# Kernel optimization log

Hardware: AMD Instinct MI355X
Metric: run time of the kernel (lower is better)

The kernel has to match this reference:

```python
import jax, jax.numpy as jnp
import numpy as np

EPS = 1e-6
K = 20
NUM_OBJECTS = 50
OBJ_FEAT = 256
C_DIM = 128
HIDDEN = 128


def vn_linear(x, W):
    # x: [B, C, 3, ...]; W: [O, C] -> [B, O, 3, ...]
    return jnp.einsum('oc,bc...->bo...', W, x)


def vn_leaky(x, Wdir, slope):
    d = vn_linear(x, Wdir)
    dot = jnp.sum(x * d, axis=2, keepdims=True)
    dsq = jnp.sum(d * d, axis=2, keepdims=True)
    x_neg = x - (dot / (dsq + EPS)) * d
    return slope * x + (1.0 - slope) * jnp.where(dot >= 0, x, x_neg)


def vn_linear_leaky(x, Wfeat, Wdir, slope):
    pf = vn_linear(x, Wfeat)
    d = vn_linear(x, Wdir)
    dot = jnp.sum(pf * d, axis=2, keepdims=True)
    dsq = jnp.sum(d * d, axis=2, keepdims=True)
    p_neg = pf - (dot / (dsq + EPS)) * d
    return slope * pf + (1.0 - slope) * jnp.where(dot >= 0, pf, p_neg)


def resblock(x, fc0, fc1, a0, a1, sc):
    net = vn_linear(vn_leaky(x, a0, 0.0), fc0)
    dx = vn_linear(vn_leaky(net, a1, 0.0), fc1)
    return vn_linear(x, sc) + dx


def get_graph_feature_cross(x, k):
    # x: [B, 3, N] -> edge features [B, 3, 3, N, k]
    inner = -2.0 * jnp.einsum('bdn,bdm->bnm', x, x)
    xx = jnp.sum(x * x, axis=1)                       # [B, N]
    neg_dist = -xx[:, :, None] - inner - xx[:, None, :]  # [B, N, N]
    idx = jax.lax.top_k(neg_dist, k)[1]               # [B, N, k] nearest neighbors
    xt = jnp.transpose(x, (0, 2, 1))                  # [B, N, 3]
    nbr = jax.vmap(lambda pts, ind: pts[ind])(xt, idx)  # [B, N, k, 3]
    ctr = jnp.broadcast_to(xt[:, :, None, :], nbr.shape)
    cross = jnp.cross(nbr, ctr)
    feat = jnp.stack([nbr - ctr, ctr, cross], axis=3)  # [B, N, k, 3, 3]
    return jnp.transpose(feat, (0, 3, 4, 1, 2))


def mlp2(zf, w0, w1, w2):
    h = jax.nn.relu(zf @ w0.T)
    h = jax.nn.relu(h @ w1.T)
    return h @ w2.T


def setup_inputs():
    key = jax.random.key(0)
    ks = jax.random.split(key, 24)
    B, N = 4, 4096

    def rn(k, shape):
        return jax.random.normal(k, shape, dtype=jnp.float32) * (1.0 / np.sqrt(shape[-1]))

    return {
        'p': jax.random.normal(ks[0], (B, N, 3), dtype=jnp.float32),
        'z_idxs': jax.random.randint(ks[1], (B,), 0, NUM_OBJECTS),
        'z': jax.random.normal(ks[2], (NUM_OBJECTS, OBJ_FEAT), dtype=jnp.float32),
        'hw0': rn(ks[3], (OBJ_FEAT, OBJ_FEAT)),
        'hw1': rn(ks[4], (OBJ_FEAT, OBJ_FEAT)),
        'hw2': rn(ks[5], (C_DIM * HIDDEN, OBJ_FEAT)),
        'hb0': rn(ks[6], (OBJ_FEAT, OBJ_FEAT)),
        'hb1': rn(ks[7], (OBJ_FEAT, OBJ_FEAT)),
        'hb2': rn(ks[8], (C_DIM, OBJ_FEAT)),
        'conv_pos_feat': rn(ks[9], (128, 3)),
        'conv_pos_dir': rn(ks[10], (128, 3)),
        'fc_pos_w': rn(ks[11], (2 * HIDDEN, 128)),
        'blk_fc0': rn(ks[12], (5, HIDDEN, 2 * HIDDEN)),
        'blk_fc1': rn(ks[13], (5, HIDDEN, HIDDEN)),
        'blk_act0': rn(ks[14], (5, 2 * HIDDEN, 2 * HIDDEN)),
        'blk_act1': rn(ks[15], (5, HIDDEN, HIDDEN)),
        'blk_sc': rn(ks[16], (5, HIDDEN, 2 * HIDDEN)),
        'actc_dir': rn(ks[17], (HIDDEN, HIDDEN)),
    }


def reference(p, z_idxs, z, hw0, hw1, hw2, hb0, hb1, hb2, conv_pos_feat,
              conv_pos_dir, fc_pos_w, blk_fc0, blk_fc1, blk_act0, blk_act1,
              blk_sc, actc_dir):
    B = p.shape[0]
    x = jnp.transpose(p, (0, 2, 1))                       # [B, 3, N]
    feat = get_graph_feature_cross(x, K)                  # [B, 3, 3, N, k]
    net = vn_linear_leaky(feat, conv_pos_feat, conv_pos_dir, 0.2)  # [B,128,3,N,k]
    net = jnp.mean(net, axis=-1)                          # [B,128,3,N]
    net = vn_linear(net, fc_pos_w)                        # [B,256,3,N]
    for i in range(5):
        net = resblock(net, blk_fc0[i], blk_fc1[i], blk_act0[i], blk_act1[i], blk_sc[i])
        if i < 4:
            pooled = jnp.mean(net, axis=-1, keepdims=True)
            net = jnp.concatenate([net, jnp.broadcast_to(pooled, net.shape)], axis=1)
    net = vn_leaky(jnp.mean(net, axis=-1), actc_dir, 0.2)  # [B, HIDDEN, 3]
    zf = z[z_idxs]                                        # [B, OBJ_FEAT]
    w = mlp2(zf, hw0, hw1, hw2).reshape(B, C_DIM, HIDDEN)  # hypernet weights
    b = mlp2(zf, hb0, hb1, hb2)                           # [B, C_DIM]
    c = jnp.einsum('bhd,bch->bcd', net, w) + b[:, :, None]  # [B, C_DIM, 3]
    return c
```

## Files before the change

### kernel.cpp

```cpp
#include <hip/hip_runtime.h>
#include <hip/hip_fp16.h>
#include <cstdint>
#include <cstddef>

#define NPTS 4096
#define BATCH 4
#define KNN 20

typedef __half f16;
using f32x4 = __attribute__((ext_vector_type(4))) float;
using f16x8 = __attribute__((ext_vector_type(8))) _Float16;

__global__ __launch_bounds__(256) void knn_kernel(const float* __restrict__ p,
                                                  int* __restrict__ idx_out) {
    __shared__ float pts[12288];
    const int tid  = threadIdx.x;
    const int wave = tid >> 6, lane = tid & 63;
    const int b  = blockIdx.x >> 10;
    const int nb = ((blockIdx.x & 1023) << 2) + wave;

    const float4* src4 = (const float4*)(p + (size_t)b * NPTS * 3);
    float4* dst4 = (float4*)pts;
    for (int i = tid; i < NPTS * 3 / 4; i += 256) dst4[i] = src4[i];
    __syncthreads();

    const float cx = pts[3 * nb], cy = pts[3 * nb + 1], cz = pts[3 * nb + 2];
    unsigned lst[4];
#pragma unroll
    for (int i = 0; i < 4; i++) lst[i] = 0xFFFFFFFFu;

    for (int t = 0; t < NPTS / 64; t++) {
        int m = (t << 6) + lane;
        float dx = pts[3 * m] - cx, dy = pts[3 * m + 1] - cy, dz = pts[3 * m + 2] - cz;
        float d = dx * dx + dy * dy + dz * dz;
        unsigned c = (__float_as_uint(d) & 0xFFFFF000u) | (unsigned)m;
#pragma unroll
        for (int j = 0; j < 4; j++) {
            unsigned lo = min(c, lst[j]);
            c = max(c, lst[j]);
            lst[j] = lo;
        }
    }

    unsigned lo = 0u, hi = 0xFFFFFFFFu;
    for (int it = 0; it < 32; it++) {
        unsigned mid = lo + ((hi - lo) >> 1);
        int cnt = __popcll(__ballot(lst[0] <= mid)) + __popcll(__ballot(lst[1] <= mid))
                + __popcll(__ballot(lst[2] <= mid)) + __popcll(__ballot(lst[3] <= mid));
        if (cnt >= KNN) hi = mid; else lo = mid + 1;
    }
    const unsigned T = hi;

    unsigned long long bl[4];
#pragma unroll
    for (int j = 0; j < 4; j++) bl[j] = __ballot(lst[j] <= T);
    const unsigned long long lmask = (lane == 63) ? ~0ull >> 1 : (1ull << lane) - 1;
    int base = 0;
    const size_t out_base = ((size_t)b * NPTS + nb) * KNN;
#pragma unroll
    for (int j = 0; j < 4; j++) {
        if (lst[j] <= T) {
            int pos = base + (int)__popcll(bl[j] & lmask);
            idx_out[out_base + pos] = (int)(lst[j] & 0xFFFu);
        }
        base += (int)__popcll(bl[j]);
    }
}

__global__ __launch_bounds__(128) void edgeconv_kernel(
    const float* __restrict__ p, const int* __restrict__ idx,
    const float* __restrict__ wf, const float* __restrict__ wd,
    f16* __restrict__ out) {
    __shared__ float e[KNN][6];
    const int col = blockIdx.x;
    const int b = col >> 12;
    const int tid = threadIdx.x;
    const float cx = p[(size_t)col * 3], cy = p[(size_t)col * 3 + 1], cz = p[(size_t)col * 3 + 2];
    if (tid < KNN) {
        int j = idx[(size_t)col * KNN + tid];
        const float* q = &p[((size_t)b * NPTS + j) * 3];
        float nx = q[0], ny = q[1], nz = q[2];
        e[tid][0] = nx - cx; e[tid][1] = ny - cy; e[tid][2] = nz - cz;
        e[tid][3] = ny * cz - nz * cy;
        e[tid][4] = nz * cx - nx * cz;
        e[tid][5] = nx * cy - ny * cx;
    }
    __syncthreads();
    const int o = tid;
    const float f0 = wf[o * 3], f1 = wf[o * 3 + 1], f2 = wf[o * 3 + 2];
    const float g0 = wd[o * 3], g1 = wd[o * 3 + 1], g2 = wd[o * 3 + 2];
    const float pc0 = f1 * cx, pc1 = f1 * cy, pc2 = f1 * cz;
    const float gc0 = g1 * cx, gc1 = g1 * cy, gc2 = g1 * cz;
    float a0 = 0.f, a1 = 0.f, a2 = 0.f;
    for (int k = 0; k < KNN; k++) {
        float d0 = e[k][0], d1 = e[k][1], d2 = e[k][2];
        float c0 = e[k][3], c1 = e[k][4], c2 = e[k][5];
        float pf0 = fmaf(f0, d0, fmaf(f2, c0, pc0));
        float pf1 = fmaf(f0, d1, fmaf(f2, c1, pc1));
        float pf2 = fmaf(f0, d2, fmaf(f2, c2, pc2));
        float dd0 = fmaf(g0, d0, fmaf(g2, c0, gc0));
        float dd1 = fmaf(g0, d1, fmaf(g2, c1, gc1));
        float dd2 = fmaf(g0, d2, fmaf(g2, c2, gc2));
        float dot = pf0 * dd0 + pf1 * dd1 + pf2 * dd2;
        float dsq = dd0 * dd0 + dd1 * dd1 + dd2 * dd2;
        float w = 0.8f * dot * __builtin_amdgcn_rcpf(dsq + 1e-6f);
        w = (dot >= 0.f) ? 0.f : w;
        a0 += pf0 - w * dd0;
        a1 += pf1 - w * dd1;
        a2 += pf2 - w * dd2;
    }
    const float inv = 1.f / (float)KNN;
    out[((size_t)col * 3 + 0) * 128 + o] = __float2half(a0 * inv);
    out[((size_t)col * 3 + 1) * 128 + o] = __float2half(a1 * inv);
    out[((size_t)col * 3 + 2) * 128 + o] = __float2half(a2 * inv);
}

template <int KIN>
__global__ __launch_bounds__(256) void resblock_kernel(
    const uint16_t* __restrict__ INg,
    const uint16_t* __restrict__ Wfcp,
    const uint16_t* __restrict__ Wa0,
    const uint16_t* __restrict__ Wfc0,
    const uint16_t* __restrict__ Wa1,
    const uint16_t* __restrict__ Wsc,
    const uint16_t* __restrict__ Wfc1,
    const float* __restrict__ PBg,
    const float* __restrict__ BAg,
    const float* __restrict__ BSCg,
    f16* __restrict__ OUTg,
    float* __restrict__ PPg) {
    constexpr int XRB  = (KIN == 256) ? 528 : 272;
    constexpr int H0RB = 528;
    constexpr int MRB  = 272;
    constexpr int MBSZ = (KIN == 256) ? 48 * 272 : 0;
    constexpr int XSZ  = 48 * XRB;
    constexpr int PBSZ = (KIN == 128) ? 1536 : 0;
    constexpr int H0O  = MBSZ + XSZ + PBSZ;
    constexpr int MIDO = H0O + 48 * H0RB;
    __shared__ char lds[MIDO + 48 * MRB];
    char* MBs = lds;
    char* INs = lds + MBSZ;
    float* PBs = (float*)(lds + MBSZ + XSZ);
    char* H0  = lds + H0O;
    char* MID = lds + MIDO;

    const int tid = threadIdx.x;
    const int lane = tid & 63;
    const int wc = tid >> 6;
    const int gr0 = blockIdx.x * 48;
    const int b = blockIdx.x >> 8;

    if (KIN == 128) {
        for (int i = tid; i < 384; i += 256) PBs[i] = PBg[b * 384 + i];
    }
    {
        char* dst = (KIN == 256) ? MBs : INs;
#pragma unroll
        for (int j = 0; j < 3; j++) {
            int chunk = tid + j * 256;
            int row = chunk >> 4, c16 = chunk & 15;
            f16x8 v = *(const f16x8*)(INg + (size_t)(gr0 + row) * 128 + c16 * 8);
            *(f16x8*)(dst + row * 272 + c16 * 16) = v;
        }
    }
    __syncthreads();

    if (KIN == 256) {
        f32x4 acc[3][4];
#pragma unroll
        for (int i = 0; i < 3; i++)
#pragma unroll
            for (int j = 0; j < 4; j++) acc[i][j] = (f32x4){0.f, 0.f, 0.f, 0.f};
#pragma unroll
        for (int ks = 0; ks < 4; ks++) {
            const int kb = ks * 64 + (lane >> 4) * 16;
            f16x8 af[3], bf[4];
#pragma unroll
            for (int mi = 0; mi < 3; mi++) {
                int r = mi * 16 + (lane & 15);
                af[mi] = *(const f16x8*)(MBs + r * 272 + kb);
            }
#pragma unroll
            for (int ni = 0; ni < 4; ni++) {
                int o = wc * 64 + ni * 16 + (lane & 15);
                bf[ni] = *(const f16x8*)(Wfcp + o * 128 + ks * 32 + (lane >> 4) * 8);
            }
#pragma unroll
            for (int mi = 0; mi < 3; mi++)
#pragma unroll
                for (int ni = 0; ni < 4; ni++)
                    acc[mi][ni] = __builtin_amdgcn_mfma_f32_16x16x32_f16(
                        af[mi], bf[ni], acc[mi][ni], 0, 0, 0);
        }
#pragma unroll
        for (int mi = 0; mi < 3; mi++)
#pragma unroll
            for (int ni = 0; ni < 4; ni++) {
                int col = wc * 64 + ni * 16 + (lane & 15);
#pragma unroll
                for (int r = 0; r < 4; r++) {
                    int row = mi * 16 + (lane >> 4) * 4 + r;
                    *(f16*)(INs + row * XRB + col * 2) = __float2half(acc[mi][ni][r]);
                }
            }
        __syncthreads();
    }

    f32x4 accS[3][2];
#pragma unroll
    for (int i = 0; i < 3; i++) { accS[i][0] = (f32x4){0,0,0,0}; accS[i][1] = (f32x4){0,0,0,0}; }
    {
        f32x4 acc[3][4];
#pragma unroll
        for (int i = 0; i < 3; i++)
#pragma unroll
            for (int j = 0; j < 4; j++) acc[i][j] = (f32x4){0.f, 0.f, 0.f, 0.f};
#pragma unroll
        for (int ks = 0; ks < KIN / 32; ks++) {
            const int kb = ks * 64 + (lane >> 4) * 16;
            f16x8 af[3], bf[4], bs[2];
#pragma unroll
            for (int mi = 0; mi < 3; mi++) {
                int r = mi * 16 + (lane & 15);
                af[mi] = *(const f16x8*)(INs + r * XRB + kb);
            }
#pragma unroll
            for (int ni = 0; ni < 4; ni++) {
                int o = wc * 64 + ni * 16 + (lane & 15);
                bf[ni] = *(const f16x8*)(Wa0 + o * 256 + ks * 32 + (lane >> 4) * 8);
            }
#pragma unroll
            for (int ni = 0; ni < 2; ni++) {
                int o = wc * 32 + ni * 16 + (lane & 15);
                bs[ni] = *(const f16x8*)(Wsc + o * 256 + ks * 32 + (lane >> 4) * 8);
            }
#pragma unroll
            for (int mi = 0; mi < 3; mi++) {
#pragma unroll
                for (int ni = 0; ni < 4; ni++)
                    acc[mi][ni] = __builtin_amdgcn_mfma_f32_16x16x32_f16(
                        af[mi], bf[ni], acc[mi][ni], 0, 0, 0);
#pragma unroll
                for (int ni = 0; ni < 2; ni++)
                    accS[mi][ni] = __builtin_amdgcn_mfma_f32_16x16x32_f16(
                        af[mi], bs[ni], accS[mi][ni], 0, 0, 0);
            }
        }
#pragma unroll
        for (int mi = 0; mi < 3; mi++)
#pragma unroll
            for (int ni = 0; ni < 4; ni++) {
                int col = wc * 64 + ni * 16 + (lane & 15);
#pragma unroll
                for (int r = 0; r < 4; r++) {
                    int row = mi * 16 + (lane >> 4) * 4 + r;
                    float v = acc[mi][ni][r];
                    if (KIN == 128) v += BAg[b * 768 + (row % 3) * 256 + col];
                    *(f16*)(H0 + row * H0RB + col * 2) = __float2half(v);
                }
            }
    }
    __syncthreads();
#pragma unroll
    for (int j = 0; j < 8; j++) {
        int it = tid + j * 256;
        int pnt = it >> 7, cp = it & 127;
        float xv[3][2], dv[3][2];
#pragma unroll
        for (int s = 0; s < 3; s++) {
            int row = pnt * 3 + s;
            __half2 d2 = *(const __half2*)(H0 + row * H0RB + cp * 4);
            dv[s][0] = __half2float(d2.x); dv[s][1] = __half2float(d2.y);
            if (KIN == 256) {
                __half2 x2 = *(const __half2*)(INs + row * XRB + cp * 4);
                xv[s][0] = __half2float(x2.x); xv[s][1] = __half2float(x2.y);
            } else {
                if (cp < 64) {
                    __half2 x2 = *(const __half2*)(INs + row * XRB + cp * 4);
                    xv[s][0] = __half2float(x2.x); xv[s][1] = __half2float(x2.y);
                } else {
                    xv[s][0] = PBs[s * 128 + (cp - 64) * 2];
                    xv[s][1] = PBs[s * 128 + (cp - 64) * 2 + 1];
                }
            }
        }
#pragma unroll
        for (int jj = 0; jj < 2; jj++) {
            float dot = xv[0][jj] * dv[0][jj] + xv[1][jj] * dv[1][jj] + xv[2][jj] * dv[2][jj];
            float dsq = dv[0][jj] * dv[0][jj] + dv[1][jj] * dv[1][jj] + dv[2][jj] * dv[2][jj];
            float coef = dot * __builtin_amdgcn_rcpf(dsq + 1e-6f);
            bool pos = dot >= 0.f;
#pragma unroll
            for (int s = 0; s < 3; s++)
                xv[s][jj] = pos ? xv[s][jj] : xv[s][jj] - coef * dv[s][jj];
        }
#pragma unroll
        for (int s = 0; s < 3; s++) {
            int row = pnt * 3 + s;
            __half2 h2;
            h2.x = __float2half(xv[s][0]);
            h2.y = __float2half(xv[s][1]);
            *(__half2*)(H0 + row * H0RB + cp * 4) = h2;
        }
    }
    __syncthreads();

    {
        f32x4 acc[3][2];
#pragma unroll
        for (int i = 0; i < 3; i++) { acc[i][0] = (f32x4){0,0,0,0}; acc[i][1] = (f32x4){0,0,0,0}; }
#pragma unroll
        for (int ks = 0; ks < 8; ks++) {
            const int kb = ks * 64 + (lane >> 4) * 16;
            f16x8 af[3], bf[2];
#pragma unroll
            for (int mi = 0; mi < 3; mi++) {
                int r = mi * 16 + (lane & 15);
                af[mi] = *(const f16x8*)(H0 + r * H0RB + kb);
            }
#pragma unroll
            for (int ni = 0; ni < 2; ni++) {
                int o = wc * 32 + ni * 16 + (lane & 15);
                bf[ni] = *(const f16x8*)(Wfc0 + o * 256 + ks * 32 + (lane >> 4) * 8);
            }
#pragma unroll
            for (int mi = 0; mi < 3; mi++)
#pragma unroll
                for (int ni = 0; ni < 2; ni++)
                    acc[mi][ni] = __builtin_amdgcn_mfma_f32_16x16x32_f16(
                        af[mi], bf[ni], acc[mi][ni], 0, 0, 0);
        }
#pragma unroll
        for (int mi = 0; mi < 3; mi++)
#pragma unroll
            for (int ni = 0; ni < 2; ni++) {
                int col = wc * 32 + ni * 16 + (lane & 15);
#pragma unroll
                for (int r = 0; r < 4; r++) {
                    int row = mi * 16 + (lane >> 4) * 4 + r;
                    *(f16*)(MID + row * MRB + col * 2) = __float2half(acc[mi][ni][r]);
                }
            }
    }
    __syncthreads();

    {
        f32x4 acc[3][2];
#pragma unroll
        for (int i = 0; i < 3; i++) { acc[i][0] = (f32x4){0,0,0,0}; acc[i][1] = (f32x4){0,0,0,0}; }
#pragma unroll
        for (int ks = 0; ks < 4; ks++) {
            const int kb = ks * 64 + (lane >> 4) * 16;
            f16x8 af[3], bf[2];
#pragma unroll
            for (int mi = 0; mi < 3; mi++) {
                int r = mi * 16 + (lane & 15);
                af[mi] = *(const f16x8*)(MID + r * MRB + kb);
            }
#pragma unroll
            for (int ni = 0; ni < 2; ni++) {
                int o = wc * 32 + ni * 16 + (lane & 15);
                bf[ni] = *(const f16x8*)(Wa1 + o * 128 + ks * 32 + (lane >> 4) * 8);
            }
#pragma unroll
            for (int mi = 0; mi < 3; mi++)
#pragma unroll
                for (int ni = 0; ni < 2; ni++)
                    acc[mi][ni] = __builtin_amdgcn_mfma_f32_16x16x32_f16(
                        af[mi], bf[ni], acc[mi][ni], 0, 0, 0);
        }
#pragma unroll
        for (int mi = 0; mi < 3; mi++)
#pragma unroll
            for (int ni = 0; ni < 2; ni++) {
                int col = wc * 32 + ni * 16 + (lane & 15);
#pragma unroll
                for (int r = 0; r < 4; r++) {
                    int row = mi * 16 + (lane >> 4) * 4 + r;
                    *(f16*)(H0 + row * MRB + col * 2) = __float2half(acc[mi][ni][r]);
                }
            }
    }
    __syncthreads();
#pragma unroll
    for (int j = 0; j < 4; j++) {
        int it = tid + j * 256;
        int pnt = it >> 6, cp = it & 63;
        float xv[3][2], dv[3][2];
#pragma unroll
        for (int s = 0; s < 3; s++) {
            int row = pnt * 3 + s;
            __half2 d2 = *(const __half2*)(H0 + row * MRB + cp * 4);
            __half2 x2 = *(const __half2*)(MID + row * MRB + cp * 4);
            dv[s][0] = __half2float(d2.x); dv[s][1] = __half2float(d2.y);
            xv[s][0] = __half2float(x2.x); xv[s][1] = __half2float(x2.y);
        }
#pragma unroll
        for (int jj = 0; jj < 2; jj++) {
            float dot = xv[0][jj] * dv[0][jj] + xv[1][jj] * dv[1][jj] + xv[2][jj] * dv[2][jj];
            float dsq = dv[0][jj] * dv[0][jj] + dv[1][jj] * dv[1][jj] + dv[2][jj] * dv[2][jj];
            float coef = dot * __builtin_amdgcn_rcpf(dsq + 1e-6f);
            bool pos = dot >= 0.f;
#pragma unroll
            for (int s = 0; s < 3; s++)
                xv[s][jj] = pos ? xv[s][jj] : xv[s][jj] - coef * dv[s][jj];
        }
#pragma unroll
        for (int s = 0; s < 3; s++) {
            int row = pnt * 3 + s;
            __half2 h2;
            h2.x = __float2half(xv[s][0]);
            h2.y = __float2half(xv[s][1]);
            *(__half2*)(H0 + row * MRB + cp * 4) = h2;
        }
    }
    __syncthreads();

    {
#pragma unroll
        for (int ks = 0; ks < 4; ks++) {
            const int kb = ks * 64 + (lane >> 4) * 16;
            f16x8 af[3], bf[2];
#pragma unroll
            for (int mi = 0; mi < 3; mi++) {
                int r = mi * 16 + (lane & 15);
                af[mi] = *(const f16x8*)(H0 + r * MRB + kb);
            }
#pragma unroll
            for (int ni = 0; ni < 2; ni++) {
                int o = wc * 32 + ni * 16 + (lane & 15);
                bf[ni] = *(const f16x8*)(Wfc1 + o * 128 + ks * 32 + (lane >> 4) * 8);
            }
#pragma unroll
            for (int mi = 0; mi < 3; mi++)
#pragma unroll
                for (int ni = 0; ni < 2; ni++)
                    accS[mi][ni] = __builtin_amdgcn_mfma_f32_16x16x32_f16(
                        af[mi], bf[ni], accS[mi][ni], 0, 0, 0);
        }
        float ps[2][3] = {};
#pragma unroll
        for (int mi = 0; mi < 3; mi++)
#pragma unroll
            for (int ni = 0; ni < 2; ni++) {
                int col = wc * 32 + ni * 16 + (lane & 15);
#pragma unroll
                for (int r = 0; r < 4; r++) {
                    int row = mi * 16 + (lane >> 4) * 4 + r;
                    float v = accS[mi][ni][r];
                    if (KIN == 128) v += BSCg[b * 384 + (row % 3) * 128 + col];
                    OUTg[(size_t)(gr0 + row) * 128 + col] = __float2half(v);
                    ps[ni][row % 3] += v;
                }
            }
#pragma unroll
        for (int ni = 0; ni < 2; ni++)
#pragma unroll
            for (int s = 0; s < 3; s++) {
                float x = ps[ni][s];
                x += __shfl_xor(x, 16, 64);
                x += __shfl_xor(x, 32, 64);
                ps[ni][s] = x;
            }
        if ((lane >> 4) == 0) {
#pragma unroll
            for (int ni = 0; ni < 2; ni++) {
                int col = wc * 32 + ni * 16 + (lane & 15);
#pragma unroll
                for (int s = 0; s < 3; s++)
                    PPg[(size_t)blockIdx.x * 384 + s * 128 + col] = ps[ni][s];
            }
        }
    }
}

__global__ __launch_bounds__(512) void poolbias_kernel(
    const float* __restrict__ PP, const f16* __restrict__ a0n, const f16* __restrict__ scn,
    float* __restrict__ PB, float* __restrict__ BA, float* __restrict__ BSC, int hasbias) {
    __shared__ float red[4][128];
    __shared__ float pl[128];
    const int bs = blockIdx.x;
    const int b = bs / 3, s = bs % 3;
    const int t = threadIdx.x;
    const int col = t & 127, seg = t >> 7;
    {
        float acc = 0.f;
        const float* base = PP + (size_t)(b * 256) * 384 + s * 128 + col;
        for (int k = seg * 64; k < seg * 64 + 64; k++) acc += base[(size_t)k * 384];
        red[seg][col] = acc;
    }
    __syncthreads();
    if (t < 128) {
        float a = (red[0][t] + red[1][t]) + (red[2][t] + red[3][t]);
        a *= (1.f / (float)NPTS);
        pl[t] = a;
        PB[bs * 128 + t] = a;
    }
    __syncthreads();
    if (!hasbias) return;
    if (t < 256) {
        float s2 = 0.f;
        for (int c = 0; c < 128; c++) s2 += __half2float(a0n[t * 256 + 128 + c]) * pl[c];
        BA[bs * 256 + t] = s2;
    } else if (t < 384) {
        int o = t - 256;
        float s2 = 0.f;
        for (int c = 0; c < 128; c++) s2 += __half2float(scn[o * 256 + 128 + c]) * pl[c];
        BSC[bs * 128 + o] = s2;
    }
}

__global__ void cvt_all(const float* __restrict__ fcpw, const float* __restrict__ act0,
                        const float* __restrict__ fc0, const float* __restrict__ act1,
                        const float* __restrict__ fc1, const float* __restrict__ scw,
                        f16* o_fcpw, f16* o_act0, f16* o_fc0, f16* o_act1, f16* o_fc1,
                        f16* o_scw) {
    int i = blockIdx.x * 256 + threadIdx.x;
    if (i < 32768) { o_fcpw[i] = __float2half(fcpw[i]); }
    else if (i < 360448) { int j = i - 32768;  o_act0[j] = __float2half(act0[j]); }
    else if (i < 524288) { int j = i - 360448; o_fc0[j]  = __float2half(fc0[j]); }
    else if (i < 606208) { int j = i - 524288; o_act1[j] = __float2half(act1[j]); }
    else if (i < 688128) { int j = i - 606208; o_fc1[j]  = __float2half(fc1[j]); }
    else                 { int j = i - 688128; o_scw[j]  = __float2half(scw[j]); }
}

__global__ __launch_bounds__(256) void hypermlp_kernel(
    const float* __restrict__ z, const int* __restrict__ zidx,
    const float* __restrict__ hw0, const float* __restrict__ hw1,
    const float* __restrict__ hb0, const float* __restrict__ hb1,
    const float* __restrict__ hb2,
    float* __restrict__ H2, float* __restrict__ BV) {
    __shared__ float zf[256], ta[256], tb[256];
    const int b = blockIdx.x, o = threadIdx.x;
    zf[o] = z[(size_t)zidx[b] * 256 + o];
    __syncthreads();
    float s = 0.f;
    for (int c = 0; c < 256; c++) s += zf[c] * hw0[o * 256 + c];
    ta[o] = fmaxf(s, 0.f);
    __syncthreads();
    s = 0.f;
    for (int c = 0; c < 256; c++) s += ta[c] * hw1[o * 256 + c];
    tb[o] = fmaxf(s, 0.f);
    __syncthreads();
    H2[(size_t)b * 256 + o] = tb[o];
    s = 0.f;
    for (int c = 0; c < 256; c++) s += zf[c] * hb0[o * 256 + c];
    __syncthreads();
    ta[o] = fmaxf(s, 0.f);
    __syncthreads();
    s = 0.f;
    for (int c = 0; c < 256; c++) s += ta[c] * hb1[o * 256 + c];
    __syncthreads();
    tb[o] = fmaxf(s, 0.f);
    __syncthreads();
    if (o < 128) {
        s = 0.f;
        for (int c = 0; c < 256; c++) s += tb[c] * hb2[o * 256 + c];
        BV[(size_t)b * 128 + o] = s;
    }
}

__global__ __launch_bounds__(256) void wmat_kernel(const float* __restrict__ H2,
                                                   const float* __restrict__ hw2,
                                                   float* __restrict__ WM) {
    __shared__ float h[256];
    const int b = blockIdx.y;
    const int row = blockIdx.x * 256 + threadIdx.x;
    h[threadIdx.x] = H2[(size_t)b * 256 + threadIdx.x];
    __syncthreads();
    float s = 0.f;
    for (int c = 0; c < 256; c++) s += h[c] * hw2[(size_t)row * 256 + c];
    WM[(size_t)b * 16384 + row] = s;
}

__global__ __launch_bounds__(384) void final_out_kernel(
    const float* __restrict__ pb, const float* __restrict__ actc,
    const float* __restrict__ WM, const float* __restrict__ BV,
    float* __restrict__ out) {
    __shared__ float pb2s[3][128];
    const int b = blockIdx.x;
    const int t = threadIdx.x;
    if (t < 128) {
        const int o = t;
        float d0 = 0.f, d1 = 0.f, d2 = 0.f;
        for (int c = 0; c < 128; c++) {
            float w = actc[o * 128 + c];
            d0 += w * pb[(size_t)(b * 3 + 0) * 128 + c];
            d1 += w * pb[(size_t)(b * 3 + 1) * 128 + c];
            d2 += w * pb[(size_t)(b * 3 + 2) * 128 + c];
        }
        float x0 = pb[(size_t)(b * 3 + 0) * 128 + o];
        float x1 = pb[(size_t)(b * 3 + 1) * 128 + o];
        float x2 = pb[(size_t)(b * 3 + 2) * 128 + o];
        float dot = x0 * d0 + x1 * d1 + x2 * d2;
        float dsq = d0 * d0 + d1 * d1 + d2 * d2;
        float coef = dot / (dsq + 1e-6f);
        bool pos = dot >= 0.f;
        float h0 = pos ? x0 : x0 - coef * d0;
        float h1 = pos ? x1 : x1 - coef * d1;
        float h2 = pos ? x2 : x2 - coef * d2;
        pb2s[0][o] = 0.2f * x0 + 0.8f * h0;
        pb2s[1][o] = 0.2f * x1 + 0.8f * h1;
        pb2s[2][o] = 0.2f * x2 + 0.8f * h2;
    }
    __syncthreads();
    const int cd = t / 3, d = t % 3;
    float s = BV[(size_t)b * 128 + cd];
    for (int h = 0; h < 128; h++)
        s += pb2s[d][h] * WM[(size_t)b * 16384 + cd * 128 + h];
    out[(size_t)b * 384 + cd * 3 + d] = s;
}

extern "C" void kernel_launch(void* const* d_in, const int* in_sizes, int n_in,
                              void* d_out, int out_size, void* d_ws, size_t ws_size,
                              hipStream_t stream) {
    (void)in_sizes; (void)n_in; (void)out_size; (void)ws_size;
    const float* p     = (const float*)d_in[0];
    const int*   zidx  = (const int*)d_in[1];
    const float* z     = (const float*)d_in[2];
    const float* hw0   = (const float*)d_in[3];
    const float* hw1   = (const float*)d_in[4];
    const float* hw2   = (const float*)d_in[5];
    const float* hb0   = (const float*)d_in[6];
    const float* hb1   = (const float*)d_in[7];
    const float* hb2   = (const float*)d_in[8];
    const float* cpf   = (const float*)d_in[9];
    const float* cpd   = (const float*)d_in[10];
    const float* fcpw  = (const float*)d_in[11];
    const float* fc0w  = (const float*)d_in[12];
    const float* fc1w  = (const float*)d_in[13];
    const float* act0  = (const float*)d_in[14];
    const float* act1  = (const float*)d_in[15];
    const float* scw   = (const float*)d_in[16];
    const float* actc  = (const float*)d_in[17];
    float* out = (float*)d_out;
    char* ws = (char*)d_ws;

    int*   IDX   = (int*)(ws + 0);
    f16*   MB    = (f16*)(ws + 1310720);
    f16*   MB2   = (f16*)(ws + 13893632);
    f16*   FCPW16= (f16*)(ws + 26476544);
    f16*   ACT0W = (f16*)(ws + 26542080);
    f16*   FC0W  = (f16*)(ws + 27197440);
    f16*   ACT1W = (f16*)(ws + 27525120);
    f16*   FC1W  = (f16*)(ws + 27688960);
    f16*   SCW16 = (f16*)(ws + 27852800);
    float* PP    = (float*)(ws + 28180480);
    float* PB    = (float*)(ws + 29753344);
    float* H2    = (float*)(ws + 29759488);
    float* BV    = (float*)(ws + 29763584);
    float* WM    = (float*)(ws + 29765632);
    float* BA    = (float*)(ws + 30027776);
    float* BSC   = (float*)(ws + 30040064);

    cvt_all<<<3328, 256, 0, stream>>>(fcpw, act0, fc0w, act1, fc1w, scw,
                                      FCPW16, ACT0W, FC0W, ACT1W, FC1W, SCW16);

    knn_kernel<<<BATCH * NPTS / 4, 256, 0, stream>>>(p, IDX);
    edgeconv_kernel<<<BATCH * NPTS, 128, 0, stream>>>(p, IDX, cpf, cpd, MB);

    resblock_kernel<256><<<1024, 256, 0, stream>>>(
        (const uint16_t*)MB, (const uint16_t*)FCPW16,
        (const uint16_t*)ACT0W, (const uint16_t*)FC0W,
        (const uint16_t*)ACT1W, (const uint16_t*)SCW16, (const uint16_t*)FC1W,
        nullptr, nullptr, nullptr, MB2, PP);
    poolbias_kernel<<<12, 512, 0, stream>>>(PP, ACT0W + 1 * 65536, SCW16 + 1 * 32768,
                                            PB, BA, BSC, 1);

    for (int i = 1; i < 5; i++) {
        const f16* a0h = ACT0W + (size_t)i * 256 * 256;
        const f16* sch = SCW16 + (size_t)i * 128 * 256;
        f16* in  = (i & 1) ? MB2 : MB;
        f16* ob  = (i & 1) ? MB : MB2;
        resblock_kernel<128><<<1024, 256, 0, stream>>>(
            (const uint16_t*)in, nullptr,
            (const uint16_t*)a0h,
            (const uint16_t*)(FC0W + (size_t)i * 128 * 256),
            (const uint16_t*)(ACT1W + (size_t)i * 128 * 128),
            (const uint16_t*)sch,
            (const uint16_t*)(FC1W + (size_t)i * 128 * 128),
            PB, BA, BSC, ob, PP);
        if (i < 4) {
            poolbias_kernel<<<12, 512, 0, stream>>>(
                PP, ACT0W + (size_t)(i + 1) * 65536, SCW16 + (size_t)(i + 1) * 32768,
                PB, BA, BSC, 1);
        } else {
            poolbias_kernel<<<12, 512, 0, stream>>>(PP, nullptr, nullptr, PB, BA, BSC, 0);
        }
    }

    hypermlp_kernel<<<4, 256, 0, stream>>>(z, zidx, hw0, hw1, hb0, hb1, hb2, H2, BV);
    wmat_kernel<<<dim3(64, 4), 256, 0, stream>>>(H2, hw2, WM);
    final_out_kernel<<<4, 384, 0, stream>>>(PB, actc, WM, BV, out);
}
```

Before: 424.0 us.

## Split resblock hidden dim into two halves to shrink LDS and registers

The resblock kernel now computes the 256-wide first activation direction, leaky nonlinearity and fc0 product in two 128-column halves, accumulating fc0 output across halves. This replaces the 256-wide H0 buffer with a 128-wide one, and the shortcut GEMM is fused with the fc1 GEMM in one K-concatenated loop at the end instead of being held in accumulators throughout. The aim is lower LDS footprint and register pressure so more blocks fit per CU, at the cost of extra barriers and a serialized two-pass structure.

```diff
diff --git a/kernel.cpp b/kernel.cpp
--- a/kernel.cpp
+++ b/kernel.cpp
@@ -130,19 +130,16 @@
     f16* __restrict__ OUTg,
     float* __restrict__ PPg) {
     constexpr int XRB  = (KIN == 256) ? 528 : 272;
-    constexpr int H0RB = 528;
-    constexpr int MRB  = 272;
-    constexpr int MBSZ = (KIN == 256) ? 48 * 272 : 0;
-    constexpr int XSZ  = 48 * XRB;
-    constexpr int PBSZ = (KIN == 128) ? 1536 : 0;
-    constexpr int H0O  = MBSZ + XSZ + PBSZ;
-    constexpr int MIDO = H0O + 48 * H0RB;
-    __shared__ char lds[MIDO + 48 * MRB];
+    constexpr int INS_OFF = (KIN == 256) ? 13056 : 0;
+    constexpr int H0_OFF  = (KIN == 256) ? 38400 : 14592;
+    constexpr int MID_OFF = (KIN == 256) ? 0 : 27648;
+    constexpr int LDS_SZ  = (KIN == 256) ? 51456 : 40704;
+    __shared__ char lds[LDS_SZ];
     char* MBs = lds;
-    char* INs = lds + MBSZ;
-    float* PBs = (float*)(lds + MBSZ + XSZ);
-    char* H0  = lds + H0O;
-    char* MID = lds + MIDO;
+    char* INs = lds + INS_OFF;
+    float* PBs = (float*)(lds + 13056);
+    char* H0h = lds + H0_OFF;
+    char* MID = lds + MID_OFF;
 
     const int tid = threadIdx.x;
     const int lane = tid & 63;
@@ -206,83 +203,183 @@
         __syncthreads();
     }
 
-    f32x4 accS[3][2];
-#pragma unroll
-    for (int i = 0; i < 3; i++) { accS[i][0] = (f32x4){0,0,0,0}; accS[i][1] = (f32x4){0,0,0,0}; }
-    {
-        f32x4 acc[3][4];
-#pragma unroll
-        for (int i = 0; i < 3; i++)
-#pragma unroll
-            for (int j = 0; j < 4; j++) acc[i][j] = (f32x4){0.f, 0.f, 0.f, 0.f};
-#pragma unroll
-        for (int ks = 0; ks < KIN / 32; ks++) {
+    f32x4 midAcc[3][2];
+#pragma unroll
+    for (int i = 0; i < 3; i++) { midAcc[i][0] = (f32x4){0,0,0,0}; midAcc[i][1] = (f32x4){0,0,0,0}; }
+
+#pragma unroll
+    for (int half = 0; half < 2; half++) {
+        {
+            f32x4 acc[3][2];
+#pragma unroll
+            for (int i = 0; i < 3; i++) { acc[i][0] = (f32x4){0,0,0,0}; acc[i][1] = (f32x4){0,0,0,0}; }
+#pragma unroll
+            for (int ks = 0; ks < KIN / 32; ks++) {
+                const int kb = ks * 64 + (lane >> 4) * 16;
+                f16x8 af[3], bf[2];
+#pragma unroll
+                for (int mi = 0; mi < 3; mi++) {
+                    int r = mi * 16 + (lane & 15);
+                    af[mi] = *(const f16x8*)(INs + r * XRB + kb);
+                }
+#pragma unroll
+                for (int ni = 0; ni < 2; ni++) {
+                    int o = half * 128 + wc * 32 + ni * 16 + (lane & 15);
+                    bf[ni] = *(const f16x8*)(Wa0 + o * 256 + ks * 32 + (lane >> 4) * 8);
+                }
+#pragma unroll
+                for (int mi = 0; mi < 3; mi++)
+#pragma unroll
+                    for (int ni = 0; ni < 2; ni++)
+                        acc[mi][ni] = __builtin_amdgcn_mfma_f32_16x16x32_f16(
+                            af[mi], bf[ni], acc[mi][ni], 0, 0, 0);
+            }
+#pragma unroll
+            for (int mi = 0; mi < 3; mi++)
+#pragma unroll
+                for (int ni = 0; ni < 2; ni++) {
+                    int col = wc * 32 + ni * 16 + (lane & 15);
+#pragma unroll
+                    for (int r = 0; r < 4; r++) {
+                        int row = mi * 16 + (lane >> 4) * 4 + r;
+                        float v = acc[mi][ni][r];
+                        if (KIN == 128)
+                            v += BAg[b * 768 + (row % 3) * 256 + half * 128 + col];
+                        *(f16*)(H0h + row * 272 + col * 2) = __float2half(v);
+                    }
+                }
+        }
+        __syncthreads();
+#pragma unroll
+        for (int j = 0; j < 4; j++) {
+            int it = tid + j * 256;
+            int pnt = it >> 6, cp = it & 63;
+            float xv[3][2], dv[3][2];
+#pragma unroll
+            for (int s = 0; s < 3; s++) {
+                int row = pnt * 3 + s;
+                __half2 d2 = *(const __half2*)(H0h + row * 272 + cp * 4);
+                dv[s][0] = __half2float(d2.x); dv[s][1] = __half2float(d2.y);
+                if (KIN == 256) {
+                    __half2 x2 = *(const __half2*)(INs + row * XRB + half * 256 + cp * 4);
+                    xv[s][0] = __half2float(x2.x); xv[s][1] = __half2float(x2.y);
+                } else {
+                    if (half == 0) {
+                        __half2 x2 = *(const __half2*)(INs + row * XRB + cp * 4);
+                        xv[s][0] = __half2float(x2.x); xv[s][1] = __half2float(x2.y);
+                    } else {
+                        xv[s][0] = PBs[s * 128 + cp * 2];
+                        xv[s][1] = PBs[s * 128 + cp * 2 + 1];
+                    }
+                }
+            }
+#pragma unroll
+            for (int jj = 0; jj < 2; jj++) {
+                float dot = xv[0][jj] * dv[0][jj] + xv[1][jj] * dv[1][jj] + xv[2][jj] * dv[2][jj];
+                float dsq = dv[0][jj] * dv[0][jj] + dv[1][jj] * dv[1][jj] + dv[2][jj] * dv[2][jj];
+                float coef = dot * __builtin_amdgcn_rcpf(dsq + 1e-6f);
+                bool pos = dot >= 0.f;
+#pragma unroll
+                for (int s = 0; s < 3; s++)
+                    xv[s][jj] = pos ? xv[s][jj] : xv[s][jj] - coef * dv[s][jj];
+            }
+#pragma unroll
+            for (int s = 0; s < 3; s++) {
+                int row = pnt * 3 + s;
+                __half2 h2;
+                h2.x = __float2half(xv[s][0]);
+                h2.y = __float2half(xv[s][1]);
+                *(__half2*)(H0h + row * 272 + cp * 4) = h2;
+            }
+        }
+        __syncthreads();
+#pragma unroll
+        for (int ks = 0; ks < 4; ks++) {
             const int kb = ks * 64 + (lane >> 4) * 16;
-            f16x8 af[3], bf[4], bs[2];
+            f16x8 af[3], bf[2];
 #pragma unroll
             for (int mi = 0; mi < 3; mi++) {
                 int r = mi * 16 + (lane & 15);
-                af[mi] = *(const f16x8*)(INs + r * XRB + kb);
-            }
-#pragma unroll
-            for (int ni = 0; ni < 4; ni++) {
-                int o = wc * 64 + ni * 16 + (lane & 15);
-                bf[ni] = *(const f16x8*)(Wa0 + o * 256 + ks * 32 + (lane >> 4) * 8);
+                af[mi] = *(const f16x8*)(H0h + r * 272 + kb);
             }
 #pragma unroll
             for (int ni = 0; ni < 2; ni++) {
                 int o = wc * 32 + ni * 16 + (lane & 15);
-                bs[ni] = *(const f16x8*)(Wsc + o * 256 + ks * 32 + (lane >> 4) * 8);
-            }
+                bf[ni] = *(const f16x8*)(Wfc0 + o * 256 + half * 128 + ks * 32 + (lane >> 4) * 8);
+            }
+#pragma unroll
+            for (int mi = 0; mi < 3; mi++)
+#pragma unroll
+                for (int ni = 0; ni < 2; ni++)
+                    midAcc[mi][ni] = __builtin_amdgcn_mfma_f32_16x16x32_f16(
+                        af[mi], bf[ni], midAcc[mi][ni], 0, 0, 0);
+        }
+        __syncthreads();
+    }
+
+#pragma unroll
+    for (int mi = 0; mi < 3; mi++)
+#pragma unroll
+        for (int ni = 0; ni < 2; ni++) {
+            int col = wc * 32 + ni * 16 + (lane & 15);
+#pragma unroll
+            for (int r = 0; r < 4; r++) {
+                int row = mi * 16 + (lane >> 4) * 4 + r;
+                *(f16*)(MID + row * 272 + col * 2) = __float2half(midAcc[mi][ni][r]);
+            }
+        }
+    __syncthreads();
+
+    {
+        f32x4 acc[3][2];
+#pragma unroll
+        for (int i = 0; i < 3; i++) { acc[i][0] = (f32x4){0,0,0,0}; acc[i][1] = (f32x4){0,0,0,0}; }
+#pragma unroll
+        for (int ks = 0; ks < 4; ks++) {
+            const int kb = ks * 64 + (lane >> 4) * 16;
+            f16x8 af[3], bf[2];
 #pragma unroll
             for (int mi = 0; mi < 3; mi++) {
-#pragma unroll
-                for (int ni = 0; ni < 4; ni++)
+                int r = mi * 16 + (lane & 15);
+                af[mi] = *(const f16x8*)(MID + r * 272 + kb);
+            }
+#pragma unroll
+            for (int ni = 0; ni < 2; ni++) {
+                int o = wc * 32 + ni * 16 + (lane & 15);
+                bf[ni] = *(const f16x8*)(Wa1 + o * 128 + ks * 32 + (lane >> 4) * 8);
+            }
+#pragma unroll
+            for (int mi = 0; mi < 3; mi++)
+#pragma unroll
+                for (int ni = 0; ni < 2; ni++)
                     acc[mi][ni] = __builtin_amdgcn_mfma_f32_16x16x32_f16(
                         af[mi], bf[ni], acc[mi][ni], 0, 0, 0);
-#pragma unroll
-                for (int ni = 0; ni < 2; ni++)
-                    accS[mi][ni] = __builtin_amdgcn_mfma_f32_16x16x32_f16(
-                        af[mi], bs[ni], accS[mi][ni], 0, 0, 0);
-            }
         }
 #pragma unroll
         for (int mi = 0; mi < 3; mi++)
 #pragma unroll
-            for (int ni = 0; ni < 4; ni++) {
-                int col = wc * 64 + ni * 16 + (lane & 15);
+            for (int ni = 0; ni < 2; ni++) {
+                int col = wc * 32 + ni * 16 + (lane & 15);
 #pragma unroll
                 for (int r = 0; r < 4; r++) {
                     int row = mi * 16 + (lane >> 4) * 4 + r;
-                    float v = acc[mi][ni][r];
-                    if (KIN == 128) v += BAg[b * 768 + (row % 3) * 256 + col];
-                    *(f16*)(H0 + row * H0RB + col * 2) = __float2half(v);
-                }
-            }
-    }
-    __syncthreads();
-#pragma unroll
-    for (int j = 0; j < 8; j++) {
+                    *(f16*)(H0h + row * 272 + col * 2) = __float2half(acc[mi][ni][r]);
+                }
+            }
+    }
+    __syncthreads();
+#pragma unroll
+    for (int j = 0; j < 4; j++) {
         int it = tid + j * 256;
-        int pnt = it >> 7, cp = it & 127;
+        int pnt = it >> 6, cp = it & 63;
         float xv[3][2], dv[3][2];
 #pragma unroll
         for (int s = 0; s < 3; s++) {
             int row = pnt * 3 + s;
-            __half2 d2 = *(const __half2*)(H0 + row * H0RB + cp * 4);
+            __half2 d2 = *(const __half2*)(H0h + row * 272 + cp * 4);
+            __half2 x2 = *(const __half2*)(MID + row * 272 + cp * 4);
             dv[s][0] = __half2float(d2.x); dv[s][1] = __half2float(d2.y);
-            if (KIN == 256) {
-                __half2 x2 = *(const __half2*)(INs + row * XRB + cp * 4);
-                xv[s][0] = __half2float(x2.x); xv[s][1] = __half2float(x2.y);
-            } else {
-                if (cp < 64) {
-                    __half2 x2 = *(const __half2*)(INs + row * XRB + cp * 4);
-                    xv[s][0] = __half2float(x2.x); xv[s][1] = __half2float(x2.y);
-                } else {
-                    xv[s][0] = PBs[s * 128 + (cp - 64) * 2];
-                    xv[s][1] = PBs[s * 128 + (cp - 64) * 2 + 1];
-                }
-            }
+            xv[s][0] = __half2float(x2.x); xv[s][1] = __half2float(x2.y);
         }
 #pragma unroll
         for (int jj = 0; jj < 2; jj++) {
@@ -300,7 +397,7 @@
             __half2 h2;
             h2.x = __float2half(xv[s][0]);
             h2.y = __float2half(xv[s][1]);
-            *(__half2*)(H0 + row * H0RB + cp * 4) = h2;
+            *(__half2*)(H0h + row * 272 + cp * 4) = h2;
         }
     }
     __syncthreads();
@@ -309,19 +406,36 @@
         f32x4 acc[3][2];
 #pragma unroll
         for (int i = 0; i < 3; i++) { acc[i][0] = (f32x4){0,0,0,0}; acc[i][1] = (f32x4){0,0,0,0}; }
-#pragma unroll
-        for (int ks = 0; ks < 8; ks++) {
-            const int kb = ks * 64 + (lane >> 4) * 16;
+        constexpr int NKS = (KIN + 128) / 32;
+#pragma unroll
+        for (int ks = 0; ks < NKS; ks++) {
+            const int kelem = ks * 32;
             f16x8 af[3], bf[2];
-#pragma unroll
-            for (int mi = 0; mi < 3; mi++) {
-                int r = mi * 16 + (lane & 15);
-                af[mi] = *(const f16x8*)(H0 + r * H0RB + kb);
-            }
-#pragma unroll
-            for (int ni = 0; ni < 2; ni++) {
-                int o = wc * 32 + ni * 16 + (lane & 15);
-                bf[ni] = *(const f16x8*)(Wfc0 + o * 256 + ks * 32 + (lane >> 4) * 8);
+            if (kelem < KIN) {
+                const int kb = kelem * 2 + (lane >> 4) * 16;
+#pragma unroll
+                for (int mi = 0; mi < 3; mi++) {
+                    int r = mi * 16 + (lane & 15);
+                    af[mi] = *(const f16x8*)(INs + r * XRB + kb);
+                }
+#pragma unroll
+                for (int ni = 0; ni < 2; ni++) {
+                    int o = wc * 32 + ni * 16 + (lane & 15);
+                    bf[ni] = *(const f16x8*)(Wsc + o * 256 + kelem + (lane >> 4) * 8);
+                }
+            } else {
+                const int kk = kelem - KIN;
+                const int kb = kk * 2 + (lane >> 4) * 16;
+#pragma unroll
+                for (int mi = 0; mi < 3; mi++) {
+                    int r = mi * 16 + (lane & 15);
+                    af[mi] = *(const f16x8*)(H0h + r * 272 + kb);
+                }
+#pragma unroll
+                for (int ni = 0; ni < 2; ni++) {
+                    int o = wc * 32 + ni * 16 + (lane & 15);
+                    bf[ni] = *(const f16x8*)(Wfc1 + o * 128 + kk + (lane >> 4) * 8);
+                }
             }
 #pragma unroll
             for (int mi = 0; mi < 3; mi++)
@@ -330,6 +444,7 @@
                     acc[mi][ni] = __builtin_amdgcn_mfma_f32_16x16x32_f16(
                         af[mi], bf[ni], acc[mi][ni], 0, 0, 0);
         }
+        float ps[2][3] = {};
 #pragma unroll
         for (int mi = 0; mi < 3; mi++)
 #pragma unroll
@@ -338,116 +453,7 @@
 #pragma unroll
                 for (int r = 0; r < 4; r++) {
                     int row = mi * 16 + (lane >> 4) * 4 + r;
-                    *(f16*)(MID + row * MRB + col * 2) = __float2half(acc[mi][ni][r]);
-                }
-            }
-    }
-    __syncthreads();
-
-    {
-        f32x4 acc[3][2];
-#pragma unroll
-        for (int i = 0; i < 3; i++) { acc[i][0] = (f32x4){0,0,0,0}; acc[i][1] = (f32x4){0,0,0,0}; }
-#pragma unroll
-        for (int ks = 0; ks < 4; ks++) {
-            const int kb = ks * 64 + (lane >> 4) * 16;
-            f16x8 af[3], bf[2];
-#pragma unroll
-            for (int mi = 0; mi < 3; mi++) {
-                int r = mi * 16 + (lane & 15);
-                af[mi] = *(const f16x8*)(MID + r * MRB + kb);
-            }
-#pragma unroll
-            for (int ni = 0; ni < 2; ni++) {
-                int o = wc * 32 + ni * 16 + (lane & 15);
-                bf[ni] = *(const f16x8*)(Wa1 + o * 128 + ks * 32 + (lane >> 4) * 8);
-            }
-#pragma unroll
-            for (int mi = 0; mi < 3; mi++)
-#pragma unroll
-                for (int ni = 0; ni < 2; ni++)
-                    acc[mi][ni] = __builtin_amdgcn_mfma_f32_16x16x32_f16(
-                        af[mi], bf[ni], acc[mi][ni], 0, 0, 0);
-        }
-#pragma unroll
-        for (int mi = 0; mi < 3; mi++)
-#pragma unroll
-            for (int ni = 0; ni < 2; ni++) {
-                int col = wc * 32 + ni * 16 + (lane & 15);
-#pragma unroll
-                for (int r = 0; r < 4; r++) {
-                    int row = mi * 16 + (lane >> 4) * 4 + r;
-                    *(f16*)(H0 + row * MRB + col * 2) = __float2half(acc[mi][ni][r]);
-                }
-            }
-    }
-    __syncthreads();
-#pragma unroll
-    for (int j = 0; j < 4; j++) {
-        int it = tid + j * 256;
-        int pnt = it >> 6, cp = it & 63;
-        float xv[3][2], dv[3][2];
-#pragma unroll
-        for (int s = 0; s < 3; s++) {
-            int row = pnt * 3 + s;
-            __half2 d2 = *(const __half2*)(H0 + row * MRB + cp * 4);
-            __half2 x2 = *(const __half2*)(MID + row * MRB + cp * 4);
-            dv[s][0] = __half2float(d2.x); dv[s][1] = __half2float(d2.y);
-            xv[s][0] = __half2float(x2.x); xv[s][1] = __half2float(x2.y);
-        }
-#pragma unroll
-        for (int jj = 0; jj < 2; jj++) {
-            float dot = xv[0][jj] * dv[0][jj] + xv[1][jj] * dv[1][jj] + xv[2][jj] * dv[2][jj];
-            float dsq = dv[0][jj] * dv[0][jj] + dv[1][jj] * dv[1][jj] + dv[2][jj] * dv[2][jj];
-            float coef = dot * __builtin_amdgcn_rcpf(dsq + 1e-6f);
-            bool pos = dot >= 0.f;
-#pragma unroll
-            for (int s = 0; s < 3; s++)
-                xv[s][jj] = pos ? xv[s][jj] : xv[s][jj] - coef * dv[s][jj];
-        }
-#pragma unroll
-        for (int s = 0; s < 3; s++) {
-            int row = pnt * 3 + s;
-            __half2 h2;
-            h2.x = __float2half(xv[s][0]);
-            h2.y = __float2half(xv[s][1]);
-            *(__half2*)(H0 + row * MRB + cp * 4) = h2;
-        }
-    }
-    __syncthreads();
-
-    {
-#pragma unroll
-        for (int ks = 0; ks < 4; ks++) {
-            const int kb = ks * 64 + (lane >> 4) * 16;
-            f16x8 af[3], bf[2];
-#pragma unroll
-            for (int mi = 0; mi < 3; mi++) {
-                int r = mi * 16 + (lane & 15);
-                af[mi] = *(const f16x8*)(H0 + r * MRB + kb);
-            }
-#pragma unroll
-            for (int ni = 0; ni < 2; ni++) {
-                int o = wc * 32 + ni * 16 + (lane & 15);
-                bf[ni] = *(const f16x8*)(Wfc1 + o * 128 + ks * 32 + (lane >> 4) * 8);
-            }
-#pragma unroll
-            for (int mi = 0; mi < 3; mi++)
-#pragma unroll
-                for (int ni = 0; ni < 2; ni++)
-                    accS[mi][ni] = __builtin_amdgcn_mfma_f32_16x16x32_f16(
-                        af[mi], bf[ni], accS[mi][ni], 0, 0, 0);
-        }
-        float ps[2][3] = {};
-#pragma unroll
-        for (int mi = 0; mi < 3; mi++)
-#pragma unroll
-            for (int ni = 0; ni < 2; ni++) {
-                int col = wc * 32 + ni * 16 + (lane & 15);
-#pragma unroll
-                for (int r = 0; r < 4; r++) {
-                    int row = mi * 16 + (lane >> 4) * 4 + r;
-                    float v = accS[mi][ni][r];
+                    float v = acc[mi][ni][r];
                     if (KIN == 128) v += BSCg[b * 384 + (row % 3) * 128 + col];
                     OUTg[(size_t)(gr0 + row) * 128 + col] = __float2half(v);
                     ps[ni][row % 3] += v;
```

Measured after the change: 394.4 us. -7.0%, faster.
